# Optimization experiments

Measured on AMD Instinct MI355X. Metric: run time of the kernel, lower is better.

The kernel has to match this reference:

```python
import jax, jax.numpy as jnp
import numpy as np

RMS_EPS = 1e-6


def setup_inputs() -> dict:
    key = jax.random.key(0)
    ks = jax.random.split(key, 6)
    B, S, D, F, E = 4, 2048, 1024, 4096, 8
    scale = 0.02
    return {
        "hidden_states": jax.random.normal(ks[0], (B, S, D), dtype=jnp.float32),
        "norm_weight": jnp.ones((D,), dtype=jnp.float32),
        "gate_w": jax.random.normal(ks[1], (E, D), dtype=jnp.float32) * scale,
        "w1": jax.random.normal(ks[2], (E, D, F), dtype=jnp.float32) * scale,
        "w3": jax.random.normal(ks[3], (E, D, F), dtype=jnp.float32) * scale,
        "w2": jax.random.normal(ks[4], (E, F, D), dtype=jnp.float32) * scale,
        "top_k": 2,
    }


def reference(hidden_states, norm_weight, gate_w, w1, w3, w2, top_k):
    B, S, D = hidden_states.shape
    E = gate_w.shape[0]
    # norm_fn: RMSNorm (pre-MoE norm in Mixtral block)
    x = hidden_states * jax.lax.rsqrt(jnp.mean(jnp.square(hidden_states), axis=-1, keepdims=True) + RMS_EPS)
    x = (x * norm_weight).reshape(-1, D)  # [T, D], T = B*S
    # router
    router_logits = jnp.einsum('td,ed->te', x, gate_w)  # [T, E]
    routing = jax.nn.softmax(router_logits.astype(jnp.float32), axis=-1)
    top_w, top_idx = jax.lax.top_k(routing, top_k)  # [T, k]
    top_w = top_w / jnp.sum(top_w, axis=-1, keepdims=True)
    top_w = top_w.astype(x.dtype)
    # dense-masked expert combine: tokens not routed to expert e get weight 0,
    # mathematically identical to the gather/scatter loop in the original.
    out = jnp.zeros_like(x)
    for e in range(E):  # fixed small loop over experts
        w_e = jnp.sum(jnp.where(top_idx == e, top_w, 0.0), axis=-1)  # [T]
        h = jax.nn.silu(x @ w1[e]) * (x @ w3[e])  # [T, F] SwiGLU expert
        out = out + w_e[:, None] * (h @ w2[e])
    return out.reshape(B, S, D), router_logits
```

## Files before the change

kernel.cpp:

```cpp
#include <hip/hip_runtime.h>
#include <hip/hip_bf16.h>

#define T_TOK 8192
#define D_DIM 1024
#define F_DIM 4096
#define E_NUM 8

typedef short s16x8 __attribute__((ext_vector_type(8)));
typedef float f32x4 __attribute__((ext_vector_type(4)));
typedef unsigned short u16x8 __attribute__((ext_vector_type(8)));

__device__ __forceinline__ unsigned short f2bf(float f) {
  union { float f; unsigned int u; } v; v.f = f;
  unsigned int u = v.u;
  return (unsigned short)((u + 0x7FFFu + ((u >> 16) & 1u)) >> 16);
}

__device__ __forceinline__ void async16(const void* g, void* l) {
  __builtin_amdgcn_global_load_lds((const __attribute__((address_space(1))) void*)g,
                                   (__attribute__((address_space(3))) void*)l, 16, 0, 0);
}

__global__ __launch_bounds__(256) void norm_router_kernel(
    const float* __restrict__ hs, const float* __restrict__ nw,
    const float* __restrict__ gw, unsigned short* __restrict__ xb,
    float* __restrict__ logits_out, int* __restrict__ cnt,
    int* __restrict__ ilist, float* __restrict__ wlist) {
  int t = blockIdx.x;
  int tid = threadIdx.x;
  int lane = tid & 63, wid = tid >> 6;
  float4 v = ((const float4*)(hs + (size_t)t * D_DIM))[tid];
  float ss = v.x * v.x + v.y * v.y + v.z * v.z + v.w * v.w;
#pragma unroll
  for (int o = 32; o > 0; o >>= 1) ss += __shfl_xor(ss, o);
  __shared__ float red[4];
  __shared__ float pl[4][8];
  if (lane == 0) red[wid] = ss;
  __syncthreads();
  float ms = (red[0] + red[1] + red[2] + red[3]) * (1.0f / 1024.0f);
  float rs = rsqrtf(ms + 1e-6f);
  float4 wv = ((const float4*)nw)[tid];
  float x0 = v.x * rs * wv.x, x1 = v.y * rs * wv.y;
  float x2 = v.z * rs * wv.z, x3 = v.w * rs * wv.w;
  ((ushort4*)(xb + (size_t)t * D_DIM))[tid] =
      make_ushort4(f2bf(x0), f2bf(x1), f2bf(x2), f2bf(x3));
  float p[8];
#pragma unroll
  for (int e = 0; e < 8; ++e) {
    float4 g = ((const float4*)(gw + (size_t)e * D_DIM))[tid];
    p[e] = x0 * g.x + x1 * g.y + x2 * g.z + x3 * g.w;
  }
#pragma unroll
  for (int e = 0; e < 8; ++e) {
#pragma unroll
    for (int o = 32; o > 0; o >>= 1) p[e] += __shfl_xor(p[e], o);
  }
  if (lane == 0) {
#pragma unroll
    for (int e = 0; e < 8; ++e) pl[wid][e] = p[e];
  }
  __syncthreads();
  if (tid == 0) {
    float l[8];
#pragma unroll
    for (int e = 0; e < 8; ++e) {
      l[e] = pl[0][e] + pl[1][e] + pl[2][e] + pl[3][e];
      logits_out[(size_t)t * 8 + e] = l[e];
    }
    int i0 = 0; float b0 = l[0];
#pragma unroll
    for (int e = 1; e < 8; ++e) if (l[e] > b0) { b0 = l[e]; i0 = e; }
    int i1 = (i0 == 0) ? 1 : 0; float b1 = l[i1];
#pragma unroll
    for (int e = 0; e < 8; ++e) if (e != i0 && l[e] > b1) { b1 = l[e]; i1 = e; }
    float wa = 1.0f / (1.0f + __expf(b1 - b0));
    float wb = 1.0f / (1.0f + __expf(b0 - b1));
    int p0 = atomicAdd(&cnt[i0], 1);
    ilist[i0 * T_TOK + p0] = t * 2;     wlist[i0 * T_TOK + p0] = wa;
    int p1 = atomicAdd(&cnt[i1], 1);
    ilist[i1 * T_TOK + p1] = t * 2 + 1; wlist[i1 * T_TOK + p1] = wb;
  }
}

__global__ __launch_bounds__(256) void transpose_cvt_kernel(
    const float* __restrict__ w1, const float* __restrict__ w3,
    const float* __restrict__ w2, unsigned short* __restrict__ w13t,
    unsigned short* __restrict__ w2t) {
  __shared__ unsigned short tileS[64][72];
  int bx = blockIdx.x;
  int tensor = bx >> 13;
  int e = (bx >> 10) & 7;
  int tl = bx & 1023;
  const float* src; int C, tr, tc;
  if (tensor == 0) {
    src = w1 + (size_t)e * D_DIM * F_DIM; C = F_DIM; tr = tl >> 6; tc = tl & 63;
  } else if (tensor == 1) {
    src = w3 + (size_t)e * D_DIM * F_DIM; C = F_DIM; tr = tl >> 6; tc = tl & 63;
  } else {
    src = w2 + (size_t)e * F_DIM * D_DIM; C = D_DIM; tr = tl >> 4; tc = tl & 15;
  }
  int r0 = tr * 64, c0 = tc * 64;
  int tid = threadIdx.x;
  int rr = tid >> 4, ccb = (tid & 15) * 4;
#pragma unroll
  for (int i = 0; i < 4; ++i) {
    int r = rr + i * 16;
    float4 v = *(const float4*)(src + (size_t)(r0 + r) * C + c0 + ccb);
    tileS[ccb + 0][r] = f2bf(v.x);
    tileS[ccb + 1][r] = f2bf(v.y);
    tileS[ccb + 2][r] = f2bf(v.z);
    tileS[ccb + 3][r] = f2bf(v.w);
  }
  __syncthreads();
  int row = tid >> 2, col = (tid & 3) * 16;
  unsigned short* dp;
  if (tensor < 2) {
    int f = c0 + row;
    int prow = ((f >> 5) * 64) + (f & 31) + (tensor == 1 ? 32 : 0);
    dp = w13t + ((size_t)e * 8192 + prow) * D_DIM + r0 + col;
  } else {
    dp = w2t + ((size_t)e * D_DIM + c0 + row) * F_DIM + r0 + col;
  }
  u16x8 v0, v1;
#pragma unroll
  for (int j = 0; j < 8; ++j) { v0[j] = tileS[row][col + j]; v1[j] = tileS[row][col + 8 + j]; }
  *(u16x8*)dp = v0;
  *(u16x8*)(dp + 8) = v1;
}

#define MFMA4(AI_, M_)                                                           \
  acc[M_][0] = __builtin_amdgcn_mfma_f32_16x16x32_bf16(AI_, b0, acc[M_][0], 0, 0, 0); \
  acc[M_][1] = __builtin_amdgcn_mfma_f32_16x16x32_bf16(AI_, b1, acc[M_][1], 0, 0, 0); \
  acc[M_][2] = __builtin_amdgcn_mfma_f32_16x16x32_bf16(AI_, b2, acc[M_][2], 0, 0, 0); \
  acc[M_][3] = __builtin_amdgcn_mfma_f32_16x16x32_bf16(AI_, b3, acc[M_][3], 0, 0, 0);

#define PHASE_TAIL()                                                             \
  __builtin_amdgcn_s_barrier();                                                  \
  asm volatile("s_waitcnt lgkmcnt(0)" ::: "memory");                             \
  __builtin_amdgcn_sched_barrier(0);                                             \
  __builtin_amdgcn_s_setprio(1);

#define PHASE_END()                                                              \
  __builtin_amdgcn_s_setprio(0);                                                 \
  __builtin_amdgcn_s_barrier();

#define G_ITER(CUR_, NXT_, KT1_, DOST_)                                          \
  {                                                                              \
    const unsigned short* Ac = &As[CUR_][0];                                     \
    const unsigned short* Bc = &Bs[CUR_][0];                                     \
    s16x8 a0, a1, a2, a3, b0, b1, b2, b3;                                        \
                                         \
    a0 = *(const s16x8*)(Ac + aoff[0]); a1 = *(const s16x8*)(Ac + aoff[1]);      \
    a2 = *(const s16x8*)(Ac + aoff[2]); a3 = *(const s16x8*)(Ac + aoff[3]);      \
    b0 = *(const s16x8*)(Bc + boff[0]); b1 = *(const s16x8*)(Bc + boff[1]);      \
    b2 = *(const s16x8*)(Bc + boff[2]); b3 = *(const s16x8*)(Bc + boff[3]);      \
    if (DOST_) {                                                                 \
      int ko = (KT1_) * 64;                                                      \
      async16(ap0 + ko, &As[NXT_][tid * 8]);                                     \
      async16(ap1 + ko, &As[NXT_][4096 + tid * 8]);                              \
      async16(ap2 + ko, &As[NXT_][8192 + tid * 8]);                              \
      async16(ap3 + ko, &As[NXT_][12288 + tid * 8]);                             \
    }                                                                            \
    PHASE_TAIL()                                                                 \
    MFMA4(a0, 0) MFMA4(a1, 1) MFMA4(a2, 2) MFMA4(a3, 3)                          \
    PHASE_END()                                                                  \
                                               \
    a0 = *(const s16x8*)(Ac + aoff[4]); a1 = *(const s16x8*)(Ac + aoff[5]);      \
    a2 = *(const s16x8*)(Ac + aoff[6]); a3 = *(const s16x8*)(Ac + aoff[7]);      \
    if (DOST_) {                                                                 \
      int ko = (KT1_) * 64;                                                      \
      async16(bp0 + ko, &Bs[NXT_][tid * 8]);                                     \
      async16(bp1 + ko, &Bs[NXT_][4096 + tid * 8]);                              \
      async16(bp2 + ko, &Bs[NXT_][8192 + tid * 8]);                              \
      async16(bp3 + ko, &Bs[NXT_][12288 + tid * 8]);                             \
    }                                                                            \
    PHASE_TAIL()                                                                 \
    MFMA4(a0, 4) MFMA4(a1, 5) MFMA4(a2, 6) MFMA4(a3, 7)                          \
    PHASE_END()                                                                  \
                                                       \
    a0 = *(const s16x8*)(Ac + (aoff[0] ^ 32)); a1 = *(const s16x8*)(Ac + (aoff[1] ^ 32)); \
    a2 = *(const s16x8*)(Ac + (aoff[2] ^ 32)); a3 = *(const s16x8*)(Ac + (aoff[3] ^ 32)); \
    b0 = *(const s16x8*)(Bc + (boff[0] ^ 32)); b1 = *(const s16x8*)(Bc + (boff[1] ^ 32)); \
    b2 = *(const s16x8*)(Bc + (boff[2] ^ 32)); b3 = *(const s16x8*)(Bc + (boff[3] ^ 32)); \
    PHASE_TAIL()                                                                 \
    MFMA4(a0, 0) MFMA4(a1, 1) MFMA4(a2, 2) MFMA4(a3, 3)                          \
    PHASE_END()                                                                  \
                \
    a0 = *(const s16x8*)(Ac + (aoff[4] ^ 32)); a1 = *(const s16x8*)(Ac + (aoff[5] ^ 32)); \
    a2 = *(const s16x8*)(Ac + (aoff[6] ^ 32)); a3 = *(const s16x8*)(Ac + (aoff[7] ^ 32)); \
    PHASE_TAIL()                                                                 \
    MFMA4(a0, 4) MFMA4(a1, 5) MFMA4(a2, 6) MFMA4(a3, 7)                          \
    __builtin_amdgcn_s_setprio(0);                                               \
    asm volatile("s_waitcnt vmcnt(0)" ::: "memory");                             \
    __builtin_amdgcn_s_barrier();                                                \
  }

__global__ __launch_bounds__(512, 2) void gemm1_kernel(
    const unsigned short* __restrict__ xb, const unsigned short* __restrict__ w13t,
    unsigned short* __restrict__ H, const int* __restrict__ cnt,
    const int* __restrict__ ilist) {
  int flat = blockIdx.x;
  int e = flat & 7;
  int work = flat >> 3;
  int rt = work & 31;
  int ft = work >> 5;
  int ne = cnt[e];
  int r0 = rt * 256;
  if (r0 >= ne) return;
  __shared__ __align__(16) unsigned short As[2][16384];
  __shared__ __align__(16) unsigned short Bs[2][16384];
  __shared__ int toks[256];
  int tid = threadIdx.x, lane = tid & 63, w = tid >> 6;
  if (tid < 256) toks[tid] = ilist[e * T_TOK + min(r0 + tid, ne - 1)];
  __syncthreads();
  const unsigned short* bpanel = w13t + ((size_t)e * 8192 + ft * 256) * D_DIM;
  int rr = tid >> 3, ch = tid & 7;
  int coff = ((ch ^ (rr & 7)) * 8);
  const unsigned short* ap0 = xb + (size_t)(toks[rr] >> 1) * D_DIM + coff;
  const unsigned short* ap1 = xb + (size_t)(toks[64 + rr] >> 1) * D_DIM + coff;
  const unsigned short* ap2 = xb + (size_t)(toks[128 + rr] >> 1) * D_DIM + coff;
  const unsigned short* ap3 = xb + (size_t)(toks[192 + rr] >> 1) * D_DIM + coff;
  const unsigned short* bp0 = bpanel + (size_t)rr * D_DIM + coff;
  const unsigned short* bp1 = bpanel + (size_t)(64 + rr) * D_DIM + coff;
  const unsigned short* bp2 = bpanel + (size_t)(128 + rr) * D_DIM + coff;
  const unsigned short* bp3 = bpanel + (size_t)(192 + rr) * D_DIM + coff;
  int wr = w >> 2, wc = w & 3;
  int lr = lane & 15, lc = lane >> 4;
  int aoff[8], boff[4];
#pragma unroll
  for (int m = 0; m < 8; ++m) {
    int row = wr * 128 + m * 16 + lr;
    aoff[m] = row * 64 + ((lc ^ (row & 7)) * 8);
  }
#pragma unroll
  for (int n = 0; n < 4; ++n) {
    int row = wc * 64 + n * 16 + lr;
    boff[n] = row * 64 + ((lc ^ (row & 7)) * 8);
  }
  f32x4 acc[8][4] = {};
  async16(ap0, &As[0][tid * 8]);       async16(ap1, &As[0][4096 + tid * 8]);
  async16(ap2, &As[0][8192 + tid * 8]); async16(ap3, &As[0][12288 + tid * 8]);
  async16(bp0, &Bs[0][tid * 8]);       async16(bp1, &Bs[0][4096 + tid * 8]);
  async16(bp2, &Bs[0][8192 + tid * 8]); async16(bp3, &Bs[0][12288 + tid * 8]);
  asm volatile("s_waitcnt vmcnt(0)" ::: "memory");
  __builtin_amdgcn_s_barrier();
  for (int kt = 0; kt < 14; kt += 2) {
    G_ITER(0, 1, kt + 1, 1)
    G_ITER(1, 0, kt + 2, 1)
  }
  G_ITER(0, 1, 15, 1)
  G_ITER(1, 0, 16, 0)

  int g4 = lane >> 4, cl = lane & 15;
  int fbase = (4 * ft + wc) * 32;
#pragma unroll
  for (int m = 0; m < 8; ++m) {
#pragma unroll
    for (int j = 0; j < 4; ++j) {
      int rloc = wr * 128 + m * 16 + g4 * 4 + j;
      if (r0 + rloc < ne) {
        unsigned short* hp = H + (size_t)toks[rloc] * F_DIM + fbase + cl;
#pragma unroll
        for (int n = 0; n < 2; ++n) {
          float c1 = acc[m][n][j], c3 = acc[m][n + 2][j];
          float h = c1 / (1.0f + __expf(-c1)) * c3;
          hp[n * 16] = f2bf(h);
        }
      }
    }
  }
}

__global__ __launch_bounds__(512, 2) void gemm2_kernel(
    const unsigned short* __restrict__ H, const unsigned short* __restrict__ w2t,
    const int* __restrict__ cnt, const int* __restrict__ ilist,
    const float* __restrict__ wlist, float* __restrict__ out) {
  int flat = blockIdx.x;
  int e = flat & 7;
  int work = flat >> 3;
  int rt = work & 31;
  int nt = work >> 5;
  int ne = cnt[e];
  int r0 = rt * 256;
  if (r0 >= ne) return;
  __shared__ __align__(16) unsigned short As[2][16384];
  __shared__ __align__(16) unsigned short Bs[2][16384];
  __shared__ int toks[256];
  __shared__ float wts[256];
  int tid = threadIdx.x, lane = tid & 63, w = tid >> 6;
  if (tid < 256) {
    int idx = e * T_TOK + min(r0 + tid, ne - 1);
    toks[tid] = ilist[idx];
    wts[tid] = wlist[idx];
  }
  __syncthreads();
  const unsigned short* bpanel = w2t + ((size_t)e * D_DIM + nt * 256) * F_DIM;
  int rr = tid >> 3, ch = tid & 7;
  int coff = ((ch ^ (rr & 7)) * 8);
  const unsigned short* ap0 = H + (size_t)toks[rr] * F_DIM + coff;
  const unsigned short* ap1 = H + (size_t)toks[64 + rr] * F_DIM + coff;
  const unsigned short* ap2 = H + (size_t)toks[128 + rr] * F_DIM + coff;
  const unsigned short* ap3 = H + (size_t)toks[192 + rr] * F_DIM + coff;
  const unsigned short* bp0 = bpanel + (size_t)rr * F_DIM + coff;
  const unsigned short* bp1 = bpanel + (size_t)(64 + rr) * F_DIM + coff;
  const unsigned short* bp2 = bpanel + (size_t)(128 + rr) * F_DIM + coff;
  const unsigned short* bp3 = bpanel + (size_t)(192 + rr) * F_DIM + coff;
  int wr = w >> 2, wc = w & 3;
  int lr = lane & 15, lc = lane >> 4;
  int aoff[8], boff[4];
#pragma unroll
  for (int m = 0; m < 8; ++m) {
    int row = wr * 128 + m * 16 + lr;
    aoff[m] = row * 64 + ((lc ^ (row & 7)) * 8);
  }
#pragma unroll
  for (int n = 0; n < 4; ++n) {
    int row = wc * 64 + n * 16 + lr;
    boff[n] = row * 64 + ((lc ^ (row & 7)) * 8);
  }
  f32x4 acc[8][4] = {};
  async16(ap0, &As[0][tid * 8]);       async16(ap1, &As[0][4096 + tid * 8]);
  async16(ap2, &As[0][8192 + tid * 8]); async16(ap3, &As[0][12288 + tid * 8]);
  async16(bp0, &Bs[0][tid * 8]);       async16(bp1, &Bs[0][4096 + tid * 8]);
  async16(bp2, &Bs[0][8192 + tid * 8]); async16(bp3, &Bs[0][12288 + tid * 8]);
  asm volatile("s_waitcnt vmcnt(0)" ::: "memory");
  __builtin_amdgcn_s_barrier();
  for (int kt = 0; kt < 62; kt += 2) {
    G_ITER(0, 1, kt + 1, 1)
    G_ITER(1, 0, kt + 2, 1)
  }
  G_ITER(0, 1, 63, 1)
  G_ITER(1, 0, 64, 0)

  int g4 = lane >> 4, cl = lane & 15;
#pragma unroll
  for (int m = 0; m < 8; ++m) {
#pragma unroll
    for (int j = 0; j < 4; ++j) {
      int rloc = wr * 128 + m * 16 + g4 * 4 + j;
      if (r0 + rloc < ne) {
        int tok = toks[rloc] >> 1;
        float ww = wts[rloc];
        float* op = out + (size_t)tok * D_DIM + nt * 256 + wc * 64 + cl;
#pragma unroll
        for (int n = 0; n < 4; ++n)
          unsafeAtomicAdd(op + n * 16, ww * acc[m][n][j]);
      }
    }
  }
}

extern "C" void kernel_launch(void* const* d_in, const int* in_sizes, int n_in,
                              void* d_out, int out_size, void* d_ws, size_t ws_size,
                              hipStream_t stream) {
  const float* hs = (const float*)d_in[0];
  const float* nw = (const float*)d_in[1];
  const float* gw = (const float*)d_in[2];
  const float* w1 = (const float*)d_in[3];
  const float* w3 = (const float*)d_in[4];
  const float* w2 = (const float*)d_in[5];
  float* out = (float*)d_out;
  float* logits_out = out + (size_t)T_TOK * D_DIM;

  char* ws = (char*)d_ws;
  unsigned short* xb   = (unsigned short*)(ws);
  unsigned short* w13t = (unsigned short*)(ws + 16777216ull);
  unsigned short* w2t  = (unsigned short*)(ws + 150994944ull);
  unsigned short* H    = (unsigned short*)(ws + 218103808ull);
  int*   ilist = (int*)(ws + 352321536ull);
  float* wlist = (float*)(ws + 352583680ull);
  int*   cnt   = (int*)(ws + 352845824ull);

  hipMemsetAsync(d_out, 0, (size_t)out_size * sizeof(float), stream);
  hipMemsetAsync(cnt, 0, E_NUM * sizeof(int), stream);
  norm_router_kernel<<<T_TOK, 256, 0, stream>>>(hs, nw, gw, xb, logits_out, cnt, ilist, wlist);
  transpose_cvt_kernel<<<3 * E_NUM * 1024, 256, 0, stream>>>(w1, w3, w2, w13t, w2t);
  gemm1_kernel<<<E_NUM * 32 * 32, 512, 0, stream>>>(xb, w13t, H, cnt, ilist);
  gemm2_kernel<<<E_NUM * 32 * 4, 512, 0, stream>>>(H, w2t, cnt, ilist, wlist, out);
}
```

Baseline: 1.017 ms.

## Prefetch two K-tiles ahead and reorder LDS reads to overlap MFMA

Restructures the GEMM main loop so global-to-LDS loads run one full tile further ahead. Both buffers are prefilled and the wait becomes vmcnt(8) instead of vmcnt(0), so the next tile's loads stay in flight during the current tile's compute. Each iteration now loads all A fragments up front and overlaps the second-half LDS reads with MFMA phases. The refill of the current buffer is issued after its last LDS read, before the final MFMA block. This raises register pressure (16 fragment vectors) and depends on careful barrier and waitcnt ordering for correctness.

New measurement: 1.009 ms. No clear change (-0.8%).

```diff
diff --git a/kernel.cpp b/kernel.cpp
--- a/kernel.cpp
+++ b/kernel.cpp
@@ -134,64 +134,64 @@
   acc[M_][2] = __builtin_amdgcn_mfma_f32_16x16x32_bf16(AI_, b2, acc[M_][2], 0, 0, 0); \
   acc[M_][3] = __builtin_amdgcn_mfma_f32_16x16x32_bf16(AI_, b3, acc[M_][3], 0, 0, 0);
 
-#define PHASE_TAIL()                                                             \
-  __builtin_amdgcn_s_barrier();                                                  \
+#define LGKM0()                                                                  \
   asm volatile("s_waitcnt lgkmcnt(0)" ::: "memory");                             \
-  __builtin_amdgcn_sched_barrier(0);                                             \
-  __builtin_amdgcn_s_setprio(1);
-
-#define PHASE_END()                                                              \
-  __builtin_amdgcn_s_setprio(0);                                                 \
-  __builtin_amdgcn_s_barrier();
-
-#define G_ITER(CUR_, NXT_, KT1_, DOST_)                                          \
+  __builtin_amdgcn_sched_barrier(0);
+
+#define G_ITER(CUR_, KT2_, DOST_, VMC_)                                          \
   {                                                                              \
     const unsigned short* Ac = &As[CUR_][0];                                     \
     const unsigned short* Bc = &Bs[CUR_][0];                                     \
-    s16x8 a0, a1, a2, a3, b0, b1, b2, b3;                                        \
-                                         \
+    s16x8 a0, a1, a2, a3, a4, a5, a6, a7, b0, b1, b2, b3, c0, c1, c2, c3;        \
+                                                                         \
     a0 = *(const s16x8*)(Ac + aoff[0]); a1 = *(const s16x8*)(Ac + aoff[1]);      \
     a2 = *(const s16x8*)(Ac + aoff[2]); a3 = *(const s16x8*)(Ac + aoff[3]);      \
+    a4 = *(const s16x8*)(Ac + aoff[4]); a5 = *(const s16x8*)(Ac + aoff[5]);      \
+    a6 = *(const s16x8*)(Ac + aoff[6]); a7 = *(const s16x8*)(Ac + aoff[7]);      \
     b0 = *(const s16x8*)(Bc + boff[0]); b1 = *(const s16x8*)(Bc + boff[1]);      \
     b2 = *(const s16x8*)(Bc + boff[2]); b3 = *(const s16x8*)(Bc + boff[3]);      \
-    if (DOST_) {                                                                 \
-      int ko = (KT1_) * 64;                                                      \
-      async16(ap0 + ko, &As[NXT_][tid * 8]);                                     \
-      async16(ap1 + ko, &As[NXT_][4096 + tid * 8]);                              \
-      async16(ap2 + ko, &As[NXT_][8192 + tid * 8]);                              \
-      async16(ap3 + ko, &As[NXT_][12288 + tid * 8]);                             \
-    }                                                                            \
-    PHASE_TAIL()                                                                 \
+    __builtin_amdgcn_s_barrier();                                                \
+    LGKM0()                                                                      \
+    __builtin_amdgcn_s_setprio(1);                                               \
     MFMA4(a0, 0) MFMA4(a1, 1) MFMA4(a2, 2) MFMA4(a3, 3)                          \
-    PHASE_END()                                                                  \
-                                               \
-    a0 = *(const s16x8*)(Ac + aoff[4]); a1 = *(const s16x8*)(Ac + aoff[5]);      \
-    a2 = *(const s16x8*)(Ac + aoff[6]); a3 = *(const s16x8*)(Ac + aoff[7]);      \
-    if (DOST_) {                                                                 \
-      int ko = (KT1_) * 64;                                                      \
-      async16(bp0 + ko, &Bs[NXT_][tid * 8]);                                     \
-      async16(bp1 + ko, &Bs[NXT_][4096 + tid * 8]);                              \
-      async16(bp2 + ko, &Bs[NXT_][8192 + tid * 8]);                              \
-      async16(bp3 + ko, &Bs[NXT_][12288 + tid * 8]);                             \
-    }                                                                            \
-    PHASE_TAIL()                                                                 \
-    MFMA4(a0, 4) MFMA4(a1, 5) MFMA4(a2, 6) MFMA4(a3, 7)                          \
-    PHASE_END()                                                                  \
-                                                       \
-    a0 = *(const s16x8*)(Ac + (aoff[0] ^ 32)); a1 = *(const s16x8*)(Ac + (aoff[1] ^ 32)); \
-    a2 = *(const s16x8*)(Ac + (aoff[2] ^ 32)); a3 = *(const s16x8*)(Ac + (aoff[3] ^ 32)); \
+    __builtin_amdgcn_s_setprio(0);                                               \
+    __builtin_amdgcn_s_barrier();                                                \
+                                                                         \
+    c0 = *(const s16x8*)(Ac + (aoff[0] ^ 32)); c1 = *(const s16x8*)(Ac + (aoff[1] ^ 32)); \
+    c2 = *(const s16x8*)(Ac + (aoff[2] ^ 32)); c3 = *(const s16x8*)(Ac + (aoff[3] ^ 32)); \
+    __builtin_amdgcn_s_barrier();                                                \
+    LGKM0()                                                                      \
+    __builtin_amdgcn_s_setprio(1);                                               \
+    MFMA4(a4, 4) MFMA4(a5, 5) MFMA4(a6, 6) MFMA4(a7, 7)                          \
+    __builtin_amdgcn_s_setprio(0);                                               \
+    __builtin_amdgcn_s_barrier();                                                \
+                                                                         \
+    a4 = *(const s16x8*)(Ac + (aoff[4] ^ 32)); a5 = *(const s16x8*)(Ac + (aoff[5] ^ 32)); \
+    a6 = *(const s16x8*)(Ac + (aoff[6] ^ 32)); a7 = *(const s16x8*)(Ac + (aoff[7] ^ 32)); \
     b0 = *(const s16x8*)(Bc + (boff[0] ^ 32)); b1 = *(const s16x8*)(Bc + (boff[1] ^ 32)); \
     b2 = *(const s16x8*)(Bc + (boff[2] ^ 32)); b3 = *(const s16x8*)(Bc + (boff[3] ^ 32)); \
-    PHASE_TAIL()                                                                 \
-    MFMA4(a0, 0) MFMA4(a1, 1) MFMA4(a2, 2) MFMA4(a3, 3)                          \
-    PHASE_END()                                                                  \
+    __builtin_amdgcn_s_barrier();                                                \
+    LGKM0()                                                                      \
+    __builtin_amdgcn_s_setprio(1);                                               \
+    MFMA4(c0, 0) MFMA4(c1, 1) MFMA4(c2, 2) MFMA4(c3, 3)                          \
+    __builtin_amdgcn_s_setprio(0);                                               \
+    __builtin_amdgcn_s_barrier();                                                \
                 \
-    a0 = *(const s16x8*)(Ac + (aoff[4] ^ 32)); a1 = *(const s16x8*)(Ac + (aoff[5] ^ 32)); \
-    a2 = *(const s16x8*)(Ac + (aoff[6] ^ 32)); a3 = *(const s16x8*)(Ac + (aoff[7] ^ 32)); \
-    PHASE_TAIL()                                                                 \
-    MFMA4(a0, 4) MFMA4(a1, 5) MFMA4(a2, 6) MFMA4(a3, 7)                          \
+    if (DOST_) {                                                                 \
+      int ko = (KT2_) * 64;                                                      \
+      async16(ap0 + ko, &As[CUR_][tid * 8]);                                     \
+      async16(ap1 + ko, &As[CUR_][4096 + tid * 8]);                              \
+      async16(ap2 + ko, &As[CUR_][8192 + tid * 8]);                              \
+      async16(ap3 + ko, &As[CUR_][12288 + tid * 8]);                             \
+      async16(bp0 + ko, &Bs[CUR_][tid * 8]);                                     \
+      async16(bp1 + ko, &Bs[CUR_][4096 + tid * 8]);                              \
+      async16(bp2 + ko, &Bs[CUR_][8192 + tid * 8]);                              \
+      async16(bp3 + ko, &Bs[CUR_][12288 + tid * 8]);                             \
+    }                                                                            \
+    __builtin_amdgcn_s_setprio(1);                                               \
+    MFMA4(a4, 4) MFMA4(a5, 5) MFMA4(a6, 6) MFMA4(a7, 7)                          \
     __builtin_amdgcn_s_setprio(0);                                               \
-    asm volatile("s_waitcnt vmcnt(0)" ::: "memory");                             \
+    asm volatile("s_waitcnt vmcnt(" VMC_ ")" ::: "memory");                      \
     __builtin_amdgcn_s_barrier();                                                \
   }
 
@@ -238,18 +238,22 @@
     boff[n] = row * 64 + ((lc ^ (row & 7)) * 8);
   }
   f32x4 acc[8][4] = {};
-  async16(ap0, &As[0][tid * 8]);       async16(ap1, &As[0][4096 + tid * 8]);
+  async16(ap0, &As[0][tid * 8]);        async16(ap1, &As[0][4096 + tid * 8]);
   async16(ap2, &As[0][8192 + tid * 8]); async16(ap3, &As[0][12288 + tid * 8]);
-  async16(bp0, &Bs[0][tid * 8]);       async16(bp1, &Bs[0][4096 + tid * 8]);
+  async16(bp0, &Bs[0][tid * 8]);        async16(bp1, &Bs[0][4096 + tid * 8]);
   async16(bp2, &Bs[0][8192 + tid * 8]); async16(bp3, &Bs[0][12288 + tid * 8]);
-  asm volatile("s_waitcnt vmcnt(0)" ::: "memory");
+  async16(ap0 + 64, &As[1][tid * 8]);        async16(ap1 + 64, &As[1][4096 + tid * 8]);
+  async16(ap2 + 64, &As[1][8192 + tid * 8]); async16(ap3 + 64, &As[1][12288 + tid * 8]);
+  async16(bp0 + 64, &Bs[1][tid * 8]);        async16(bp1 + 64, &Bs[1][4096 + tid * 8]);
+  async16(bp2 + 64, &Bs[1][8192 + tid * 8]); async16(bp3 + 64, &Bs[1][12288 + tid * 8]);
+  asm volatile("s_waitcnt vmcnt(8)" ::: "memory");
   __builtin_amdgcn_s_barrier();
   for (int kt = 0; kt < 14; kt += 2) {
-    G_ITER(0, 1, kt + 1, 1)
-    G_ITER(1, 0, kt + 2, 1)
-  }
-  G_ITER(0, 1, 15, 1)
-  G_ITER(1, 0, 16, 0)
+    G_ITER(0, kt + 2, 1, "8")
+    G_ITER(1, kt + 3, 1, "8")
+  }
+  G_ITER(0, 16, 0, "0")
+  G_ITER(1, 17, 0, "0")
 
   int g4 = lane >> 4, cl = lane & 15;
   int fbase = (4 * ft + wc) * 32;
@@ -319,18 +323,22 @@
     boff[n] = row * 64 + ((lc ^ (row & 7)) * 8);
   }
   f32x4 acc[8][4] = {};
-  async16(ap0, &As[0][tid * 8]);       async16(ap1, &As[0][4096 + tid * 8]);
+  async16(ap0, &As[0][tid * 8]);        async16(ap1, &As[0][4096 + tid * 8]);
   async16(ap2, &As[0][8192 + tid * 8]); async16(ap3, &As[0][12288 + tid * 8]);
-  async16(bp0, &Bs[0][tid * 8]);       async16(bp1, &Bs[0][4096 + tid * 8]);
+  async16(bp0, &Bs[0][tid * 8]);        async16(bp1, &Bs[0][4096 + tid * 8]);
   async16(bp2, &Bs[0][8192 + tid * 8]); async16(bp3, &Bs[0][12288 + tid * 8]);
-  asm volatile("s_waitcnt vmcnt(0)" ::: "memory");
+  async16(ap0 + 64, &As[1][tid * 8]);        async16(ap1 + 64, &As[1][4096 + tid * 8]);
+  async16(ap2 + 64, &As[1][8192 + tid * 8]); async16(ap3 + 64, &As[1][12288 + tid * 8]);
+  async16(bp0 + 64, &Bs[1][tid * 8]);        async16(bp1 + 64, &Bs[1][4096 + tid * 8]);
+  async16(bp2 + 64, &Bs[1][8192 + tid * 8]); async16(bp3 + 64, &Bs[1][12288 + tid * 8]);
+  asm volatile("s_waitcnt vmcnt(8)" ::: "memory");
   __builtin_amdgcn_s_barrier();
   for (int kt = 0; kt < 62; kt += 2) {
-    G_ITER(0, 1, kt + 1, 1)
-    G_ITER(1, 0, kt + 2, 1)
-  }
-  G_ITER(0, 1, 63, 1)
-  G_ITER(1, 0, 64, 0)
+    G_ITER(0, kt + 2, 1, "8")
+    G_ITER(1, kt + 3, 1, "8")
+  }
+  G_ITER(0, 64, 0, "0")
+  G_ITER(1, 65, 0, "0")
 
   int g4 = lane >> 4, cl = lane & 15;
 #pragma unroll
```

## Split LDS tiles into halves and stage loads earlier in GEMM pipeline

Applied to the files above, without the earlier changes.

Restructures the main loop of both expert GEMM kernels so that A and B tiles are split into halves, and each half is prefetched into the double buffer at a different phase. Half of the next-next tile is issued as soon as the current half is consumed, which keeps more global loads in flight (vmcnt(4) rather than vmcnt(0)). The wave-to-row mapping is permuted into two accumulator groups so the halves free up in order, and two barrier/waitcnt points per phase are removed. The aim is to hide global-to-LDS latency behind the MFMAs, at the cost of tighter reasoning about buffer-reuse hazards.

Measured after the change: 1.043 ms. 2.6% more time.

```diff
diff --git a/kernel.cpp b/kernel.cpp
--- a/kernel.cpp
+++ b/kernel.cpp
@@ -128,71 +128,89 @@
   *(u16x8*)(dp + 8) = v1;
 }
 
-#define MFMA4(AI_, M_)                                                           \
-  acc[M_][0] = __builtin_amdgcn_mfma_f32_16x16x32_bf16(AI_, b0, acc[M_][0], 0, 0, 0); \
-  acc[M_][1] = __builtin_amdgcn_mfma_f32_16x16x32_bf16(AI_, b1, acc[M_][1], 0, 0, 0); \
-  acc[M_][2] = __builtin_amdgcn_mfma_f32_16x16x32_bf16(AI_, b2, acc[M_][2], 0, 0, 0); \
-  acc[M_][3] = __builtin_amdgcn_mfma_f32_16x16x32_bf16(AI_, b3, acc[M_][3], 0, 0, 0);
-
-#define PHASE_TAIL()                                                             \
-  __builtin_amdgcn_s_barrier();                                                  \
-  asm volatile("s_waitcnt lgkmcnt(0)" ::: "memory");                             \
-  __builtin_amdgcn_sched_barrier(0);                                             \
-  __builtin_amdgcn_s_setprio(1);
-
-#define PHASE_END()                                                              \
-  __builtin_amdgcn_s_setprio(0);                                                 \
-  __builtin_amdgcn_s_barrier();
-
-#define G_ITER(CUR_, NXT_, KT1_, DOST_)                                          \
-  {                                                                              \
-    const unsigned short* Ac = &As[CUR_][0];                                     \
-    const unsigned short* Bc = &Bs[CUR_][0];                                     \
-    s16x8 a0, a1, a2, a3, b0, b1, b2, b3;                                        \
-                                         \
-    a0 = *(const s16x8*)(Ac + aoff[0]); a1 = *(const s16x8*)(Ac + aoff[1]);      \
-    a2 = *(const s16x8*)(Ac + aoff[2]); a3 = *(const s16x8*)(Ac + aoff[3]);      \
-    b0 = *(const s16x8*)(Bc + boff[0]); b1 = *(const s16x8*)(Bc + boff[1]);      \
-    b2 = *(const s16x8*)(Bc + boff[2]); b3 = *(const s16x8*)(Bc + boff[3]);      \
-    if (DOST_) {                                                                 \
-      int ko = (KT1_) * 64;                                                      \
-      async16(ap0 + ko, &As[NXT_][tid * 8]);                                     \
-      async16(ap1 + ko, &As[NXT_][4096 + tid * 8]);                              \
-      async16(ap2 + ko, &As[NXT_][8192 + tid * 8]);                              \
-      async16(ap3 + ko, &As[NXT_][12288 + tid * 8]);                             \
-    }                                                                            \
-    PHASE_TAIL()                                                                 \
-    MFMA4(a0, 0) MFMA4(a1, 1) MFMA4(a2, 2) MFMA4(a3, 3)                          \
-    PHASE_END()                                                                  \
-                                               \
-    a0 = *(const s16x8*)(Ac + aoff[4]); a1 = *(const s16x8*)(Ac + aoff[5]);      \
-    a2 = *(const s16x8*)(Ac + aoff[6]); a3 = *(const s16x8*)(Ac + aoff[7]);      \
-    if (DOST_) {                                                                 \
-      int ko = (KT1_) * 64;                                                      \
-      async16(bp0 + ko, &Bs[NXT_][tid * 8]);                                     \
-      async16(bp1 + ko, &Bs[NXT_][4096 + tid * 8]);                              \
-      async16(bp2 + ko, &Bs[NXT_][8192 + tid * 8]);                              \
-      async16(bp3 + ko, &Bs[NXT_][12288 + tid * 8]);                             \
-    }                                                                            \
-    PHASE_TAIL()                                                                 \
-    MFMA4(a0, 4) MFMA4(a1, 5) MFMA4(a2, 6) MFMA4(a3, 7)                          \
-    PHASE_END()                                                                  \
-                                                       \
-    a0 = *(const s16x8*)(Ac + (aoff[0] ^ 32)); a1 = *(const s16x8*)(Ac + (aoff[1] ^ 32)); \
-    a2 = *(const s16x8*)(Ac + (aoff[2] ^ 32)); a3 = *(const s16x8*)(Ac + (aoff[3] ^ 32)); \
-    b0 = *(const s16x8*)(Bc + (boff[0] ^ 32)); b1 = *(const s16x8*)(Bc + (boff[1] ^ 32)); \
-    b2 = *(const s16x8*)(Bc + (boff[2] ^ 32)); b3 = *(const s16x8*)(Bc + (boff[3] ^ 32)); \
-    PHASE_TAIL()                                                                 \
-    MFMA4(a0, 0) MFMA4(a1, 1) MFMA4(a2, 2) MFMA4(a3, 3)                          \
-    PHASE_END()                                                                  \
-                \
-    a0 = *(const s16x8*)(Ac + (aoff[4] ^ 32)); a1 = *(const s16x8*)(Ac + (aoff[5] ^ 32)); \
-    a2 = *(const s16x8*)(Ac + (aoff[6] ^ 32)); a3 = *(const s16x8*)(Ac + (aoff[7] ^ 32)); \
-    PHASE_TAIL()                                                                 \
-    MFMA4(a0, 4) MFMA4(a1, 5) MFMA4(a2, 6) MFMA4(a3, 7)                          \
-    __builtin_amdgcn_s_setprio(0);                                               \
-    asm volatile("s_waitcnt vmcnt(0)" ::: "memory");                             \
-    __builtin_amdgcn_s_barrier();                                                \
+#define RD(P_, O_) (*(const s16x8*)((P_) + (O_)))
+
+#define STG_AOUT(P_, KO_)                                     \
+  async16(sa0 + (KO_), &As[P_][tid * 8]);                     \
+  async16(sa1 + (KO_), &As[P_][4096 + tid * 8]);
+#define STG_AIN(P_, KO_)                                      \
+  async16(sa2 + (KO_), &As[P_][8192 + tid * 8]);              \
+  async16(sa3 + (KO_), &As[P_][12288 + tid * 8]);
+#define STG_BH0(P_, KO_)                                      \
+  async16(sb0 + (KO_), &Bs[P_][tid * 8]);                     \
+  async16(sb1 + (KO_), &Bs[P_][4096 + tid * 8]);
+#define STG_BH1(P_, KO_)                                      \
+  async16(sb2 + (KO_), &Bs[P_][8192 + tid * 8]);              \
+  async16(sb3 + (KO_), &Bs[P_][12288 + tid * 8]);
+
+#define MF4(A_, I_, F_)                                                               \
+  A_[I_][0] = __builtin_amdgcn_mfma_f32_16x16x32_bf16(F_, b0, A_[I_][0], 0, 0, 0);    \
+  A_[I_][1] = __builtin_amdgcn_mfma_f32_16x16x32_bf16(F_, b1, A_[I_][1], 0, 0, 0);    \
+  A_[I_][2] = __builtin_amdgcn_mfma_f32_16x16x32_bf16(F_, b2, A_[I_][2], 0, 0, 0);    \
+  A_[I_][3] = __builtin_amdgcn_mfma_f32_16x16x32_bf16(F_, b3, A_[I_][3], 0, 0, 0);
+
+#define ITER(CUR_, T_, DO1_, DO4_, VMC_)                                   \
+  {                                                                        \
+    const unsigned short* Ac = &As[CUR_][0];                               \
+    const unsigned short* Bc = &Bs[CUR_][0];                               \
+    s16x8 f0, f1, f2, f3, b0, b1, b2, b3;                                  \
+                                                        \
+    f0 = RD(Ac, aG0[0]); f1 = RD(Ac, aG0[1]);                              \
+    f2 = RD(Ac, aG0[2]); f3 = RD(Ac, aG0[3]);                              \
+    b0 = RD(Bc, boff[0]); b1 = RD(Bc, boff[1]);                            \
+    b2 = RD(Bc, boff[2]); b3 = RD(Bc, boff[3]);                            \
+    if (DO1_) {                                                            \
+      int ko = ((T_) + 1) * 64;                                            \
+      STG_AIN((CUR_) ^ 1, ko) STG_BH1((CUR_) ^ 1, ko)                      \
+    }                                                                      \
+    __builtin_amdgcn_s_setprio(1);                                         \
+    MF4(acc0, 0, f0) MF4(acc0, 1, f1) MF4(acc0, 2, f2) MF4(acc0, 3, f3)    \
+    __builtin_amdgcn_s_setprio(0);                                         \
+    __builtin_amdgcn_s_barrier();                                          \
+                                                        \
+    f0 = RD(Ac, aG1[0]); f1 = RD(Ac, aG1[1]);                              \
+    f2 = RD(Ac, aG1[2]); f3 = RD(Ac, aG1[3]);                              \
+    __builtin_amdgcn_s_setprio(1);                                         \
+    MF4(acc1, 0, f0) MF4(acc1, 1, f1) MF4(acc1, 2, f2) MF4(acc1, 3, f3)    \
+    __builtin_amdgcn_s_setprio(0);                                         \
+    __builtin_amdgcn_s_barrier();                                          \
+                                                        \
+    f0 = RD(Ac, aG0[0] ^ 32); f1 = RD(Ac, aG0[1] ^ 32);                    \
+    f2 = RD(Ac, aG0[2] ^ 32); f3 = RD(Ac, aG0[3] ^ 32);                    \
+    b0 = RD(Bc, boff[0] ^ 32); b1 = RD(Bc, boff[1] ^ 32);                  \
+    b2 = RD(Bc, boff[2] ^ 32); b3 = RD(Bc, boff[3] ^ 32);                  \
+    __builtin_amdgcn_s_setprio(1);                                         \
+    MF4(acc0, 0, f0) MF4(acc0, 1, f1) MF4(acc0, 2, f2) MF4(acc0, 3, f3)    \
+    __builtin_amdgcn_s_setprio(0);                                         \
+    asm volatile("s_waitcnt lgkmcnt(0)" ::: "memory");                     \
+    __builtin_amdgcn_s_barrier();                                          \
+                                                        \
+    f0 = RD(Ac, aG1[0] ^ 32); f1 = RD(Ac, aG1[1] ^ 32);                    \
+    f2 = RD(Ac, aG1[2] ^ 32); f3 = RD(Ac, aG1[3] ^ 32);                    \
+    if (DO4_) {                                                            \
+      int ko = ((T_) + 2) * 64;                                            \
+      STG_AOUT(CUR_, ko) STG_BH0(CUR_, ko)                                 \
+    }                                                                      \
+    __builtin_amdgcn_s_setprio(1);                                         \
+    MF4(acc1, 0, f0) MF4(acc1, 1, f1) MF4(acc1, 2, f2) MF4(acc1, 3, f3)    \
+    __builtin_amdgcn_s_setprio(0);                                         \
+    asm volatile("s_waitcnt lgkmcnt(0) vmcnt(" VMC_ ")" ::: "memory");     \
+    __builtin_amdgcn_s_barrier();                                          \
+  }
+
+#define SETUP_OFFS()                                                       \
+  int wr = w >> 2, wc = w & 3;                                             \
+  int lr = lane & 15, lc = lane >> 4;                                      \
+  int aG0[4], aG1[4], boff[4];                                             \
+  _Pragma("unroll") for (int i = 0; i < 4; ++i) {                          \
+    int r = wr * 192 + i * 16 + lr;                                        \
+    aG0[i] = (r - wr * 128) * 64 + ((lc ^ (r & 7)) * 8);                   \
+    int r2 = 64 + wr * 64 + i * 16 + lr;                                   \
+    aG1[i] = (r2 + 64) * 64 + ((lc ^ (r2 & 7)) * 8);                       \
+  }                                                                        \
+  _Pragma("unroll") for (int n = 0; n < 4; ++n) {                          \
+    int r = wc * 64 + n * 16 + lr;                                         \
+    boff[n] = r * 64 + ((lc ^ (r & 7)) * 8);                               \
   }
 
 __global__ __launch_bounds__(512, 2) void gemm1_kernel(
@@ -214,57 +232,52 @@
   if (tid < 256) toks[tid] = ilist[e * T_TOK + min(r0 + tid, ne - 1)];
   __syncthreads();
   const unsigned short* bpanel = w13t + ((size_t)e * 8192 + ft * 256) * D_DIM;
-  int rr = tid >> 3, ch = tid & 7;
-  int coff = ((ch ^ (rr & 7)) * 8);
-  const unsigned short* ap0 = xb + (size_t)(toks[rr] >> 1) * D_DIM + coff;
-  const unsigned short* ap1 = xb + (size_t)(toks[64 + rr] >> 1) * D_DIM + coff;
-  const unsigned short* ap2 = xb + (size_t)(toks[128 + rr] >> 1) * D_DIM + coff;
-  const unsigned short* ap3 = xb + (size_t)(toks[192 + rr] >> 1) * D_DIM + coff;
-  const unsigned short* bp0 = bpanel + (size_t)rr * D_DIM + coff;
-  const unsigned short* bp1 = bpanel + (size_t)(64 + rr) * D_DIM + coff;
-  const unsigned short* bp2 = bpanel + (size_t)(128 + rr) * D_DIM + coff;
-  const unsigned short* bp3 = bpanel + (size_t)(192 + rr) * D_DIM + coff;
-  int wr = w >> 2, wc = w & 3;
-  int lr = lane & 15, lc = lane >> 4;
-  int aoff[8], boff[4];
-#pragma unroll
-  for (int m = 0; m < 8; ++m) {
-    int row = wr * 128 + m * 16 + lr;
-    aoff[m] = row * 64 + ((lc ^ (row & 7)) * 8);
-  }
-#pragma unroll
-  for (int n = 0; n < 4; ++n) {
-    int row = wc * 64 + n * 16 + lr;
-    boff[n] = row * 64 + ((lc ^ (row & 7)) * 8);
-  }
-  f32x4 acc[8][4] = {};
-  async16(ap0, &As[0][tid * 8]);       async16(ap1, &As[0][4096 + tid * 8]);
-  async16(ap2, &As[0][8192 + tid * 8]); async16(ap3, &As[0][12288 + tid * 8]);
-  async16(bp0, &Bs[0][tid * 8]);       async16(bp1, &Bs[0][4096 + tid * 8]);
-  async16(bp2, &Bs[0][8192 + tid * 8]); async16(bp3, &Bs[0][12288 + tid * 8]);
-  asm volatile("s_waitcnt vmcnt(0)" ::: "memory");
+  int r8 = tid >> 3;
+  int coff = (((tid & 7) ^ (r8 & 7)) * 8);
+  const unsigned short* sa0 = xb + (size_t)(toks[r8] >> 1) * D_DIM + coff;
+  const unsigned short* sa1 = xb + (size_t)(toks[r8 + 192] >> 1) * D_DIM + coff;
+  const unsigned short* sa2 = xb + (size_t)(toks[r8 + 64] >> 1) * D_DIM + coff;
+  const unsigned short* sa3 = xb + (size_t)(toks[r8 + 128] >> 1) * D_DIM + coff;
+  const unsigned short* sb0 = bpanel + (size_t)r8 * D_DIM + coff;
+  const unsigned short* sb1 = bpanel + (size_t)(r8 + 64) * D_DIM + coff;
+  const unsigned short* sb2 = bpanel + (size_t)(r8 + 128) * D_DIM + coff;
+  const unsigned short* sb3 = bpanel + (size_t)(r8 + 192) * D_DIM + coff;
+  SETUP_OFFS()
+  f32x4 acc0[4][4] = {};
+  f32x4 acc1[4][4] = {};
+  STG_AOUT(0, 0) STG_AIN(0, 0) STG_BH0(0, 0) STG_BH1(0, 0)
+  STG_AOUT(1, 64) STG_BH0(1, 64)
+  asm volatile("s_waitcnt vmcnt(4)" ::: "memory");
   __builtin_amdgcn_s_barrier();
-  for (int kt = 0; kt < 14; kt += 2) {
-    G_ITER(0, 1, kt + 1, 1)
-    G_ITER(1, 0, kt + 2, 1)
-  }
-  G_ITER(0, 1, 15, 1)
-  G_ITER(1, 0, 16, 0)
+  for (int t = 0; t <= 12; t += 2) {
+    ITER(0, t, 1, 1, "4")
+    ITER(1, t + 1, 1, 1, "4")
+  }
+  ITER(0, 14, 1, 0, "0")
+  ITER(1, 15, 0, 0, "0")
 
   int g4 = lane >> 4, cl = lane & 15;
   int fbase = (4 * ft + wc) * 32;
 #pragma unroll
-  for (int m = 0; m < 8; ++m) {
+  for (int i = 0; i < 4; ++i) {
 #pragma unroll
     for (int j = 0; j < 4; ++j) {
-      int rloc = wr * 128 + m * 16 + g4 * 4 + j;
-      if (r0 + rloc < ne) {
-        unsigned short* hp = H + (size_t)toks[rloc] * F_DIM + fbase + cl;
+      int rl0 = wr * 192 + i * 16 + g4 * 4 + j;
+      if (r0 + rl0 < ne) {
+        unsigned short* hp = H + (size_t)toks[rl0] * F_DIM + fbase + cl;
 #pragma unroll
         for (int n = 0; n < 2; ++n) {
-          float c1 = acc[m][n][j], c3 = acc[m][n + 2][j];
-          float h = c1 / (1.0f + __expf(-c1)) * c3;
-          hp[n * 16] = f2bf(h);
+          float c1 = acc0[i][n][j], c3 = acc0[i][n + 2][j];
+          hp[n * 16] = f2bf(c1 / (1.0f + __expf(-c1)) * c3);
+        }
+      }
+      int rl1 = 64 + wr * 64 + i * 16 + g4 * 4 + j;
+      if (r0 + rl1 < ne) {
+        unsigned short* hp = H + (size_t)toks[rl1] * F_DIM + fbase + cl;
+#pragma unroll
+        for (int n = 0; n < 2; ++n) {
+          float c1 = acc1[i][n][j], c3 = acc1[i][n + 2][j];
+          hp[n * 16] = f2bf(c1 / (1.0f + __expf(-c1)) * c3);
         }
       }
     }
@@ -295,56 +308,51 @@
   }
   __syncthreads();
   const unsigned short* bpanel = w2t + ((size_t)e * D_DIM + nt * 256) * F_DIM;
-  int rr = tid >> 3, ch = tid & 7;
-  int coff = ((ch ^ (rr & 7)) * 8);
-  const unsigned short* ap0 = H + (size_t)toks[rr] * F_DIM + coff;
-  const unsigned short* ap1 = H + (size_t)toks[64 + rr] * F_DIM + coff;
-  const unsigned short* ap2 = H + (size_t)toks[128 + rr] * F_DIM + coff;
-  const unsigned short* ap3 = H + (size_t)toks[192 + rr] * F_DIM + coff;
-  const unsigned short* bp0 = bpanel + (size_t)rr * F_DIM + coff;
-  const unsigned short* bp1 = bpanel + (size_t)(64 + rr) * F_DIM + coff;
-  const unsigned short* bp2 = bpanel + (size_t)(128 + rr) * F_DIM + coff;
-  const unsigned short* bp3 = bpanel + (size_t)(192 + rr) * F_DIM + coff;
-  int wr = w >> 2, wc = w & 3;
-  int lr = lane & 15, lc = lane >> 4;
-  int aoff[8], boff[4];
-#pragma unroll
-  for (int m = 0; m < 8; ++m) {
-    int row = wr * 128 + m * 16 + lr;
-    aoff[m] = row * 64 + ((lc ^ (row & 7)) * 8);
-  }
-#pragma unroll
-  for (int n = 0; n < 4; ++n) {
-    int row = wc * 64 + n * 16 + lr;
-    boff[n] = row * 64 + ((lc ^ (row & 7)) * 8);
-  }
-  f32x4 acc[8][4] = {};
-  async16(ap0, &As[0][tid * 8]);       async16(ap1, &As[0][4096 + tid * 8]);
-  async16(ap2, &As[0][8192 + tid * 8]); async16(ap3, &As[0][12288 + tid * 8]);
-  async16(bp0, &Bs[0][tid * 8]);       async16(bp1, &Bs[0][4096 + tid * 8]);
-  async16(bp2, &Bs[0][8192 + tid * 8]); async16(bp3, &Bs[0][12288 + tid * 8]);
-  asm volatile("s_waitcnt vmcnt(0)" ::: "memory");
+  int r8 = tid >> 3;
+  int coff = (((tid & 7) ^ (r8 & 7)) * 8);
+  const unsigned short* sa0 = H + (size_t)toks[r8] * F_DIM + coff;
+  const unsigned short* sa1 = H + (size_t)toks[r8 + 192] * F_DIM + coff;
+  const unsigned short* sa2 = H + (size_t)toks[r8 + 64] * F_DIM + coff;
+  const unsigned short* sa3 = H + (size_t)toks[r8 + 128] * F_DIM + coff;
+  const unsigned short* sb0 = bpanel + (size_t)r8 * F_DIM + coff;
+  const unsigned short* sb1 = bpanel + (size_t)(r8 + 64) * F_DIM + coff;
+  const unsigned short* sb2 = bpanel + (size_t)(r8 + 128) * F_DIM + coff;
+  const unsigned short* sb3 = bpanel + (size_t)(r8 + 192) * F_DIM + coff;
+  SETUP_OFFS()
+  f32x4 acc0[4][4] = {};
+  f32x4 acc1[4][4] = {};
+  STG_AOUT(0, 0) STG_AIN(0, 0) STG_BH0(0, 0) STG_BH1(0, 0)
+  STG_AOUT(1, 64) STG_BH0(1, 64)
+  asm volatile("s_waitcnt vmcnt(4)" ::: "memory");
   __builtin_amdgcn_s_barrier();
-  for (int kt = 0; kt < 62; kt += 2) {
-    G_ITER(0, 1, kt + 1, 1)
-    G_ITER(1, 0, kt + 2, 1)
-  }
-  G_ITER(0, 1, 63, 1)
-  G_ITER(1, 0, 64, 0)
+  for (int t = 0; t <= 60; t += 2) {
+    ITER(0, t, 1, 1, "4")
+    ITER(1, t + 1, 1, 1, "4")
+  }
+  ITER(0, 62, 1, 0, "0")
+  ITER(1, 63, 0, 0, "0")
 
   int g4 = lane >> 4, cl = lane & 15;
-#pragma unroll
-  for (int m = 0; m < 8; ++m) {
+  int nbase = nt * 256 + wc * 64 + cl;
+#pragma unroll
+  for (int i = 0; i < 4; ++i) {
 #pragma unroll
     for (int j = 0; j < 4; ++j) {
-      int rloc = wr * 128 + m * 16 + g4 * 4 + j;
-      if (r0 + rloc < ne) {
-        int tok = toks[rloc] >> 1;
-        float ww = wts[rloc];
-        float* op = out + (size_t)tok * D_DIM + nt * 256 + wc * 64 + cl;
+      int rl0 = wr * 192 + i * 16 + g4 * 4 + j;
+      if (r0 + rl0 < ne) {
+        float ww = wts[rl0];
+        float* op = out + (size_t)(toks[rl0] >> 1) * D_DIM + nbase;
 #pragma unroll
         for (int n = 0; n < 4; ++n)
-          unsafeAtomicAdd(op + n * 16, ww * acc[m][n][j]);
+          unsafeAtomicAdd(op + n * 16, ww * acc0[i][n][j]);
+      }
+      int rl1 = 64 + wr * 64 + i * 16 + g4 * 4 + j;
+      if (r0 + rl1 < ne) {
+        float ww = wts[rl1];
+        float* op = out + (size_t)(toks[rl1] >> 1) * D_DIM + nbase;
+#pragma unroll
+        for (int n = 0; n < 4; ++n)
+          unsafeAtomicAdd(op + n * 16, ww * acc1[i][n][j]);
       }
     }
   }
```
